# Kernel optimization log

Measured on AMD Instinct MI355X. Metric: run time of the kernel, lower is better.

The kernel has to match this reference:

```python
import jax, jax.numpy as jnp
import numpy as np

D_MODEL = 1024
NUM_HEADS = 16
BATCH = 4
SEQ = 2048


def _trunc_normal(key, shape, std):
    # truncated normal in [-3*std, 3*std], matching nn.init.trunc_normal_
    return jax.random.truncated_normal(key, -3.0, 3.0, shape, dtype=jnp.float32) * std


def setup_inputs() -> dict:
    key = jax.random.key(0)
    kx, kq, kk, kv, ko = jax.random.split(key, 5)
    std = np.sqrt(2.0 / (D_MODEL + D_MODEL)).astype(np.float32)
    x = jax.random.normal(kx, (BATCH, SEQ, D_MODEL), dtype=jnp.float32)
    # nn.Linear stores weight as [out, in]; y = x @ W.T
    W_q = _trunc_normal(kq, (D_MODEL, D_MODEL), std)
    W_k = _trunc_normal(kk, (D_MODEL, D_MODEL), std)
    W_v = _trunc_normal(kv, (D_MODEL, D_MODEL), std)
    W_o = _trunc_normal(ko, (D_MODEL, D_MODEL), std)
    return {"x": x, "W_q": W_q, "W_k": W_k, "W_v": W_v, "W_o": W_o}


def reference(x, W_q, W_k, W_v, W_o):
    b, s, d_model = x.shape
    h = NUM_HEADS
    d_k = d_model // h

    def split_heads(t):
        return t.reshape(b, s, h, d_k).transpose(0, 2, 1, 3)  # b h s d

    Q = split_heads(x @ W_q.T)
    K = split_heads(x @ W_k.T)
    V = split_heads(x @ W_v.T)

    # F.scaled_dot_product_attention with attn_mask=None -> NON-causal
    scale = 1.0 / jnp.sqrt(jnp.asarray(d_k, dtype=x.dtype))
    scores = jnp.einsum('bhqd,bhkd->bhqk', Q, K) * scale
    attn = jax.nn.softmax(scores, axis=-1)
    out = jnp.einsum('bhqk,bhkd->bhqd', attn, V)
    out = out.transpose(0, 2, 1, 3).reshape(b, s, d_model)
    return out @ W_o.T
```

## Files before the change

### kernel.cpp

```cpp
#include <hip/hip_runtime.h>
#include <hip/hip_bf16.h>
#include <stdint.h>


#define D_MODEL 1024
#define NHEAD 16
#define BATCH 4
#define SEQ 2048
#define DK 64
#define MTOT (BATCH * SEQ)

typedef __attribute__((ext_vector_type(4))) float f32x4;
typedef __attribute__((ext_vector_type(16))) float f32x16;
typedef __attribute__((ext_vector_type(8))) __bf16 bf16x8;
typedef __attribute__((ext_vector_type(8))) unsigned short ushort8;
typedef __attribute__((ext_vector_type(4))) unsigned short us4;

static __device__ __forceinline__ unsigned short f2bf(float f) {
  union { float f; unsigned int u; } v;
  v.f = f;
  unsigned int r = v.u + (0x7fffu + ((v.u >> 16) & 1u));
  return (unsigned short)(r >> 16);
}

static __device__ __forceinline__ f32x4 mfma16(bf16x8 a, bf16x8 b, f32x4 c) {
  return __builtin_amdgcn_mfma_f32_16x16x32_bf16(a, b, c, 0, 0, 0);
}
static __device__ __forceinline__ f32x16 mfma32(bf16x8 a, bf16x8 b, f32x16 c) {
  return __builtin_amdgcn_mfma_f32_32x32x16_bf16(a, b, c, 0, 0, 0);
}

static __device__ __forceinline__ unsigned int cvt_pk_bf16(float lo, float hi) {
  unsigned int r;
  asm("v_cvt_pk_bf16_f32 %0, %1, %2" : "=v"(r) : "v"(lo), "v"(hi));
  return r;
}

static __device__ __forceinline__ void gl_lds16(const void* g, void* l) {
  __builtin_amdgcn_global_load_lds((const __attribute__((address_space(1))) void*)g,
                                   (__attribute__((address_space(3))) void*)l, 16, 0, 0);
}

__global__ __launch_bounds__(256) void cvt_f32_bf16(const float* __restrict__ in,
                                                    unsigned short* __restrict__ out) {
  int i = blockIdx.x * 256 + threadIdx.x;
  f32x4 a = ((const f32x4*)in)[2 * i];
  f32x4 b = ((const f32x4*)in)[2 * i + 1];
  ushort8 r;
  r[0] = f2bf(a[0]); r[1] = f2bf(a[1]); r[2] = f2bf(a[2]); r[3] = f2bf(a[3]);
  r[4] = f2bf(b[0]); r[5] = f2bf(b[1]); r[6] = f2bf(b[2]); r[7] = f2bf(b[3]);
  ((ushort8*)out)[i] = r;
}

__global__ __launch_bounds__(256, 2) void gemm_qkv(const unsigned short* __restrict__ A,
                                                   const unsigned short* __restrict__ B3,
                                                   unsigned short* __restrict__ qh,
                                                   unsigned short* __restrict__ kh,
                                                   unsigned short* __restrict__ vtg,
                                                   float qscale) {
  __shared__ unsigned short lA[128][64];
  __shared__ unsigned short lB[128][64];
  const int t = threadIdx.x;
  const int wid = t >> 6, lane = t & 63;
  const int lr = lane & 15, lg = lane >> 4;
  const int wr = wid >> 1, wc = wid & 1;
  const int m0 = blockIdx.y * 128, n0 = blockIdx.x * 128;
  const int row8 = t >> 3, c8 = t & 7;

  f32x4 acc[4][4] = {};

  for (int kt = 0; kt < 16; ++kt) {
    const int k0 = kt * 64;
    if (kt) __syncthreads();
#pragma unroll
    for (int p = 0; p < 4; ++p) {
      gl_lds16(A  + (size_t)(m0 + p * 32 + row8) * 1024 + k0 + c8 * 8,
               &lA[0][0] + p * 2048 + t * 8);
      gl_lds16(B3 + (size_t)(n0 + p * 32 + row8) * 1024 + k0 + c8 * 8,
               &lB[0][0] + p * 2048 + t * 8);
    }
    __syncthreads();

    bf16x8 af[4][2], bfr[4][2];
#pragma unroll
    for (int rb = 0; rb < 4; ++rb)
#pragma unroll
      for (int kb = 0; kb < 2; ++kb) {
        af[rb][kb] = *(const bf16x8*)&lA[wr * 64 + rb * 16 + lr][kb * 32 + lg * 8];
        bfr[rb][kb] = *(const bf16x8*)&lB[wc * 64 + rb * 16 + lr][kb * 32 + lg * 8];
      }
    __builtin_amdgcn_s_setprio(1);
#pragma unroll
    for (int rb = 0; rb < 4; ++rb)
#pragma unroll
      for (int cb = 0; cb < 4; ++cb)
#pragma unroll
        for (int kb = 0; kb < 2; ++kb)
          acc[rb][cb] = mfma16(af[rb][kb], bfr[cb][kb], acc[rb][cb]);
    __builtin_amdgcn_s_setprio(0);
  }

  const int sel = n0 >> 10;
  const float scale = (sel == 0) ? qscale : 1.0f;
#pragma unroll
  for (int rb = 0; rb < 4; ++rb) {
    int mbase = m0 + wr * 64 + rb * 16 + lg * 4;
    int b = mbase >> 11, s0 = mbase & 2047;
#pragma unroll
    for (int cb = 0; cb < 4; ++cb) {
      int n = n0 + wc * 64 + cb * 16 + lr;
      int nl = n & 1023;
      int h = nl >> 6, d = nl & 63;
      if (sel == 2) {
        us4 v;
#pragma unroll
        for (int j = 0; j < 4; ++j) v[j] = f2bf(acc[rb][cb][j]);
        *(us4*)(vtg + ((size_t)(b * NHEAD + h) * DK + d) * SEQ + s0) = v;
      } else {
        unsigned short* out = (sel == 0) ? qh : kh;
#pragma unroll
        for (int j = 0; j < 4; ++j)
          out[((size_t)(b * NHEAD + h) * SEQ + s0 + j) * DK + d] = f2bf(acc[rb][cb][j] * scale);
      }
    }
  }
}

__global__ __launch_bounds__(256, 2) void gemm_o(const unsigned short* __restrict__ A,
                                                 const unsigned short* __restrict__ B,
                                                 float* __restrict__ out) {
  __shared__ unsigned short lA[128][64];
  __shared__ unsigned short lB[128][64];
  const int t = threadIdx.x;
  const int wid = t >> 6, lane = t & 63;
  const int lr = lane & 15, lg = lane >> 4;
  const int wr = wid >> 1, wc = wid & 1;
  const int m0 = blockIdx.y * 128, n0 = blockIdx.x * 128;
  const int row8 = t >> 3, c8 = t & 7;

  f32x4 acc[4][4] = {};

  for (int kt = 0; kt < 16; ++kt) {
    const int k0 = kt * 64;
    if (kt) __syncthreads();
#pragma unroll
    for (int p = 0; p < 4; ++p) {
      gl_lds16(A + (size_t)(m0 + p * 32 + row8) * 1024 + k0 + c8 * 8,
               &lA[0][0] + p * 2048 + t * 8);
      gl_lds16(B + (size_t)(n0 + p * 32 + row8) * 1024 + k0 + c8 * 8,
               &lB[0][0] + p * 2048 + t * 8);
    }
    __syncthreads();

    bf16x8 af[4][2], bfr[4][2];
#pragma unroll
    for (int rb = 0; rb < 4; ++rb)
#pragma unroll
      for (int kb = 0; kb < 2; ++kb) {
        af[rb][kb] = *(const bf16x8*)&lA[wr * 64 + rb * 16 + lr][kb * 32 + lg * 8];
        bfr[rb][kb] = *(const bf16x8*)&lB[wc * 64 + rb * 16 + lr][kb * 32 + lg * 8];
      }
    __builtin_amdgcn_s_setprio(1);
#pragma unroll
    for (int rb = 0; rb < 4; ++rb)
#pragma unroll
      for (int cb = 0; cb < 4; ++cb)
#pragma unroll
        for (int kb = 0; kb < 2; ++kb)
          acc[rb][cb] = mfma16(af[rb][kb], bfr[cb][kb], acc[rb][cb]);
    __builtin_amdgcn_s_setprio(0);
  }

#pragma unroll
  for (int rb = 0; rb < 4; ++rb) {
    int mbase = m0 + wr * 64 + rb * 16 + lg * 4;
#pragma unroll
    for (int cb = 0; cb < 4; ++cb) {
      int n = n0 + wc * 64 + cb * 16 + lr;
#pragma unroll
      for (int j = 0; j < 4; ++j)
        out[(size_t)(mbase + j) * 1024 + n] = acc[rb][cb][j];
    }
  }
}

__global__ __launch_bounds__(256, 2) void attn_fwd(const unsigned short* __restrict__ Qh,
                                                   const unsigned short* __restrict__ Kh,
                                                   const unsigned short* __restrict__ Vt_g,
                                                   unsigned short* __restrict__ Oout) {
  __shared__ unsigned short Kl[64 * 64];
  __shared__ unsigned short Vl[64 * 64];

  const int t = threadIdx.x;
  const int wq = t >> 6, lane = t & 63;
  const int l31 = lane & 31, hi = lane >> 5;

  const int wg = blockIdx.x;
  const int work = (wg & 7) * 64 + (wg >> 3);
  const int bh = work >> 3, qi = work & 7;
  const int q0 = qi * 256 + wq * 64;
  const size_t base = (size_t)bh * SEQ * DK;
  const int srow = t >> 3, sc = t & 7;

  bf16x8 qf0[4], qf1[4];
#pragma unroll
  for (int dt = 0; dt < 4; ++dt) {
    qf0[dt] = *(const bf16x8*)(Qh + base + (size_t)(q0 + l31) * DK + dt * 16 + hi * 8);
    qf1[dt] = *(const bf16x8*)(Qh + base + (size_t)(q0 + 32 + l31) * DK + dt * 16 + hi * 8);
  }

  f32x16 o0[2] = {}, o1[2] = {};
  float l0 = 0.f, l1 = 0.f;

  ushort8 rk0 = *(const ushort8*)(Kh + base + (size_t)srow * DK + sc * 8);
  ushort8 rk1 = *(const ushort8*)(Kh + base + (size_t)(srow + 32) * DK + sc * 8);
  ushort8 rv0 = *(const ushort8*)(Vt_g + base + (size_t)srow * SEQ + sc * 8);
  ushort8 rv1 = *(const ushort8*)(Vt_g + base + (size_t)(srow + 32) * SEQ + sc * 8);

  for (int kt = 0; kt < SEQ / 64; ++kt) {
    __syncthreads();
    {
      const int r0 = srow, r1 = srow + 32;
      *(ushort8*)((char*)Kl + ((r0 * 128 + sc * 16) ^ ((r0 & 7) << 4))) = rk0;
      *(ushort8*)((char*)Kl + ((r1 * 128 + sc * 16) ^ ((r1 & 7) << 4))) = rk1;
      *(ushort8*)((char*)Vl + ((r0 * 128 + sc * 16) ^ ((r0 & 7) << 4))) = rv0;
      *(ushort8*)((char*)Vl + ((r1 * 128 + sc * 16) ^ ((r1 & 7) << 4))) = rv1;
    }
    __syncthreads();

    if (kt < SEQ / 64 - 1) {
      const int nxt = (kt + 1) * 64;
      rk0 = *(const ushort8*)(Kh + base + (size_t)(nxt + srow) * DK + sc * 8);
      rk1 = *(const ushort8*)(Kh + base + (size_t)(nxt + srow + 32) * DK + sc * 8);
      rv0 = *(const ushort8*)(Vt_g + base + (size_t)srow * SEQ + nxt + sc * 8);
      rv1 = *(const ushort8*)(Vt_g + base + (size_t)(srow + 32) * SEQ + nxt + sc * 8);
    }

    f32x16 sS0[2] = {}, sS1[2] = {};
    __builtin_amdgcn_s_setprio(1);
#pragma unroll
    for (int kb = 0; kb < 2; ++kb) {
      const int row = kb * 32 + l31;
#pragma unroll
      for (int dt = 0; dt < 4; ++dt) {
        bf16x8 kf = *(const bf16x8*)((const char*)Kl +
                      ((row * 128 + dt * 32 + hi * 16) ^ ((row & 7) << 4)));
        sS0[kb] = mfma32(kf, qf0[dt], sS0[kb]);
        sS1[kb] = mfma32(kf, qf1[dt], sS1[kb]);
      }
    }
    __builtin_amdgcn_s_setprio(0);

    {
      float a0 = 0.f, a1 = 0.f, a2 = 0.f, a3 = 0.f;
#pragma unroll
      for (int kb = 0; kb < 2; ++kb)
#pragma unroll
        for (int r = 0; r < 16; r += 4) {
          float p0 = __builtin_amdgcn_exp2f(sS0[kb][r + 0]);
          float p1 = __builtin_amdgcn_exp2f(sS0[kb][r + 1]);
          float p2 = __builtin_amdgcn_exp2f(sS0[kb][r + 2]);
          float p3 = __builtin_amdgcn_exp2f(sS0[kb][r + 3]);
          sS0[kb][r + 0] = p0; sS0[kb][r + 1] = p1;
          sS0[kb][r + 2] = p2; sS0[kb][r + 3] = p3;
          a0 += p0; a1 += p1; a2 += p2; a3 += p3;
        }
      float ps = (a0 + a1) + (a2 + a3);
      ps += __shfl_xor(ps, 32, 64);
      l0 += ps;
    }
    {
      float a0 = 0.f, a1 = 0.f, a2 = 0.f, a3 = 0.f;
#pragma unroll
      for (int kb = 0; kb < 2; ++kb)
#pragma unroll
        for (int r = 0; r < 16; r += 4) {
          float p0 = __builtin_amdgcn_exp2f(sS1[kb][r + 0]);
          float p1 = __builtin_amdgcn_exp2f(sS1[kb][r + 1]);
          float p2 = __builtin_amdgcn_exp2f(sS1[kb][r + 2]);
          float p3 = __builtin_amdgcn_exp2f(sS1[kb][r + 3]);
          sS1[kb][r + 0] = p0; sS1[kb][r + 1] = p1;
          sS1[kb][r + 2] = p2; sS1[kb][r + 3] = p3;
          a0 += p0; a1 += p1; a2 += p2; a3 += p3;
        }
      float ps = (a0 + a1) + (a2 + a3);
      ps += __shfl_xor(ps, 32, 64);
      l1 += ps;
    }

    __builtin_amdgcn_s_setprio(1);
#pragma unroll
    for (int ks = 0; ks < 4; ++ks) {
      const int kk = ks >> 1, rb = (ks & 1) * 8;
      unsigned int a0 = cvt_pk_bf16(sS0[kk][rb + 0], sS0[kk][rb + 1]);
      unsigned int a1 = cvt_pk_bf16(sS0[kk][rb + 2], sS0[kk][rb + 3]);
      unsigned int b0 = cvt_pk_bf16(sS0[kk][rb + 4], sS0[kk][rb + 5]);
      unsigned int b1 = cvt_pk_bf16(sS0[kk][rb + 6], sS0[kk][rb + 7]);
      asm("v_permlane32_swap_b32 %0, %1" : "+v"(a0), "+v"(b0));
      asm("v_permlane32_swap_b32 %0, %1" : "+v"(a1), "+v"(b1));
      union { unsigned int u[4]; bf16x8 v; } pw0;
      pw0.u[0] = a0; pw0.u[1] = a1; pw0.u[2] = b0; pw0.u[3] = b1;

      unsigned int c0 = cvt_pk_bf16(sS1[kk][rb + 0], sS1[kk][rb + 1]);
      unsigned int c1 = cvt_pk_bf16(sS1[kk][rb + 2], sS1[kk][rb + 3]);
      unsigned int d0 = cvt_pk_bf16(sS1[kk][rb + 4], sS1[kk][rb + 5]);
      unsigned int d1 = cvt_pk_bf16(sS1[kk][rb + 6], sS1[kk][rb + 7]);
      asm("v_permlane32_swap_b32 %0, %1" : "+v"(c0), "+v"(d0));
      asm("v_permlane32_swap_b32 %0, %1" : "+v"(c1), "+v"(d1));
      union { unsigned int u[4]; bf16x8 v; } pw1;
      pw1.u[0] = c0; pw1.u[1] = c1; pw1.u[2] = d0; pw1.u[3] = d1;

#pragma unroll
      for (int dt = 0; dt < 2; ++dt) {
        const int row = dt * 32 + l31;
        bf16x8 vf = *(const bf16x8*)((const char*)Vl +
                      ((row * 128 + ks * 32 + hi * 16) ^ ((row & 7) << 4)));
        o0[dt] = mfma32(vf, pw0.v, o0[dt]);
        o1[dt] = mfma32(vf, pw1.v, o1[dt]);
      }
    }
    __builtin_amdgcn_s_setprio(0);
  }

  const int b = bh >> 4, hh = bh & 15;
  {
    const int q = q0 + l31;
    const float inv = 1.0f / l0;
    unsigned short* orow = Oout + (size_t)(b * SEQ + q) * D_MODEL + hh * 64 + hi * 4;
#pragma unroll
    for (int dt = 0; dt < 2; ++dt)
#pragma unroll
      for (int i = 0; i < 4; ++i) {
        us4 v;
#pragma unroll
        for (int j = 0; j < 4; ++j) v[j] = f2bf(o0[dt][4 * i + j] * inv);
        *(us4*)(orow + dt * 32 + 8 * i) = v;
      }
  }
  {
    const int q = q0 + 32 + l31;
    const float inv = 1.0f / l1;
    unsigned short* orow = Oout + (size_t)(b * SEQ + q) * D_MODEL + hh * 64 + hi * 4;
#pragma unroll
    for (int dt = 0; dt < 2; ++dt)
#pragma unroll
      for (int i = 0; i < 4; ++i) {
        us4 v;
#pragma unroll
        for (int j = 0; j < 4; ++j) v[j] = f2bf(o1[dt][4 * i + j] * inv);
        *(us4*)(orow + dt * 32 + 8 * i) = v;
      }
  }
}

extern "C" void kernel_launch(void* const* d_in, const int* in_sizes, int n_in,
                              void* d_out, int out_size, void* d_ws, size_t ws_size,
                              hipStream_t stream) {
  (void)in_sizes; (void)n_in; (void)out_size; (void)ws_size;
  const float* x = (const float*)d_in[0];
  const float* Wq = (const float*)d_in[1];
  const float* Wk = (const float*)d_in[2];
  const float* Wv = (const float*)d_in[3];
  const float* Wo = (const float*)d_in[4];

  char* ws = (char*)d_ws;
  unsigned short* xb   = (unsigned short*)(ws + 0);
  unsigned short* wqkv = (unsigned short*)(ws + 16777216);
  unsigned short* wob  = (unsigned short*)(ws + 23068672);
  unsigned short* qh   = (unsigned short*)(ws + 25165824);
  unsigned short* kh   = (unsigned short*)(ws + 41943040);
  unsigned short* vtg  = (unsigned short*)(ws + 58720256);
  unsigned short* at   = (unsigned short*)(ws + 75497472);

  cvt_f32_bf16<<<4096, 256, 0, stream>>>(x, xb);
  cvt_f32_bf16<<<512, 256, 0, stream>>>(Wq, wqkv);
  cvt_f32_bf16<<<512, 256, 0, stream>>>(Wk, wqkv + 1048576);
  cvt_f32_bf16<<<512, 256, 0, stream>>>(Wv, wqkv + 2097152);
  cvt_f32_bf16<<<512, 256, 0, stream>>>(Wo, wob);

  gemm_qkv<<<dim3(24, 64), 256, 0, stream>>>(xb, wqkv, qh, kh, vtg, 0.1803368801f);

  attn_fwd<<<512, 256, 0, stream>>>(qh, kh, vtg, at);

  gemm_o<<<dim3(8, 64), 256, 0, stream>>>(at, wob, (float*)d_out);
}
```

Measured before the change: 188.2 us.

## Read K/V fragments directly from global memory in attention, fuse weight conversions

Attention no longer stages K and V tiles through LDS with barriers. Each wave instead loads its MFMA fragments straight from global memory, relying on cache hits across the four waves in a block. The four weight-conversion launches become one kernel that selects its source by block index and writes into the contiguous wqkv/wob region. Both GEMMs raise their min-blocks-per-CU launch bound from 2 to 3. Dropping LDS staging removes barrier stalls, but each wave now issues redundant global loads with no software prefetch, so latency is exposed inside the inner loop.

After: 228.5 us. 1.21x slower.

```diff
diff --git a/kernel.cpp b/kernel.cpp
--- a/kernel.cpp
+++ b/kernel.cpp
@@ -52,7 +52,23 @@
   ((ushort8*)out)[i] = r;
 }
 
-__global__ __launch_bounds__(256, 2) void gemm_qkv(const unsigned short* __restrict__ A,
+__global__ __launch_bounds__(256) void cvt_w4(const float* __restrict__ wq,
+                                              const float* __restrict__ wk,
+                                              const float* __restrict__ wv,
+                                              const float* __restrict__ wo,
+                                              unsigned short* __restrict__ out) {
+  const int sel = blockIdx.x >> 9;
+  const float* in = (sel == 0) ? wq : (sel == 1) ? wk : (sel == 2) ? wv : wo;
+  int i = (blockIdx.x & 511) * 256 + threadIdx.x;
+  f32x4 a = ((const f32x4*)in)[2 * i];
+  f32x4 b = ((const f32x4*)in)[2 * i + 1];
+  ushort8 r;
+  r[0] = f2bf(a[0]); r[1] = f2bf(a[1]); r[2] = f2bf(a[2]); r[3] = f2bf(a[3]);
+  r[4] = f2bf(b[0]); r[5] = f2bf(b[1]); r[6] = f2bf(b[2]); r[7] = f2bf(b[3]);
+  ((ushort8*)(out + (size_t)sel * 1048576))[i] = r;
+}
+
+__global__ __launch_bounds__(256, 3) void gemm_qkv(const unsigned short* __restrict__ A,
                                                    const unsigned short* __restrict__ B3,
                                                    unsigned short* __restrict__ qh,
                                                    unsigned short* __restrict__ kh,
@@ -126,7 +142,7 @@
   }
 }
 
-__global__ __launch_bounds__(256, 2) void gemm_o(const unsigned short* __restrict__ A,
+__global__ __launch_bounds__(256, 3) void gemm_o(const unsigned short* __restrict__ A,
                                                  const unsigned short* __restrict__ B,
                                                  float* __restrict__ out) {
   __shared__ unsigned short lA[128][64];
@@ -188,9 +204,6 @@
                                                    const unsigned short* __restrict__ Kh,
                                                    const unsigned short* __restrict__ Vt_g,
                                                    unsigned short* __restrict__ Oout) {
-  __shared__ unsigned short Kl[64 * 64];
-  __shared__ unsigned short Vl[64 * 64];
-
   const int t = threadIdx.x;
   const int wq = t >> 6, lane = t & 63;
   const int l31 = lane & 31, hi = lane >> 5;
@@ -200,7 +213,6 @@
   const int bh = work >> 3, qi = work & 7;
   const int q0 = qi * 256 + wq * 64;
   const size_t base = (size_t)bh * SEQ * DK;
-  const int srow = t >> 3, sc = t & 7;
 
   bf16x8 qf0[4], qf1[4];
 #pragma unroll
@@ -212,39 +224,20 @@
   f32x16 o0[2] = {}, o1[2] = {};
   float l0 = 0.f, l1 = 0.f;
 
-  ushort8 rk0 = *(const ushort8*)(Kh + base + (size_t)srow * DK + sc * 8);
-  ushort8 rk1 = *(const ushort8*)(Kh + base + (size_t)(srow + 32) * DK + sc * 8);
-  ushort8 rv0 = *(const ushort8*)(Vt_g + base + (size_t)srow * SEQ + sc * 8);
-  ushort8 rv1 = *(const ushort8*)(Vt_g + base + (size_t)(srow + 32) * SEQ + sc * 8);
+  const unsigned short* Kb = Kh + base;
+  const unsigned short* Vb = Vt_g + base;
 
   for (int kt = 0; kt < SEQ / 64; ++kt) {
-    __syncthreads();
-    {
-      const int r0 = srow, r1 = srow + 32;
-      *(ushort8*)((char*)Kl + ((r0 * 128 + sc * 16) ^ ((r0 & 7) << 4))) = rk0;
-      *(ushort8*)((char*)Kl + ((r1 * 128 + sc * 16) ^ ((r1 & 7) << 4))) = rk1;
-      *(ushort8*)((char*)Vl + ((r0 * 128 + sc * 16) ^ ((r0 & 7) << 4))) = rv0;
-      *(ushort8*)((char*)Vl + ((r1 * 128 + sc * 16) ^ ((r1 & 7) << 4))) = rv1;
-    }
-    __syncthreads();
-
-    if (kt < SEQ / 64 - 1) {
-      const int nxt = (kt + 1) * 64;
-      rk0 = *(const ushort8*)(Kh + base + (size_t)(nxt + srow) * DK + sc * 8);
-      rk1 = *(const ushort8*)(Kh + base + (size_t)(nxt + srow + 32) * DK + sc * 8);
-      rv0 = *(const ushort8*)(Vt_g + base + (size_t)srow * SEQ + nxt + sc * 8);
-      rv1 = *(const ushort8*)(Vt_g + base + (size_t)(srow + 32) * SEQ + nxt + sc * 8);
-    }
+    const int s0 = kt * 64;
 
     f32x16 sS0[2] = {}, sS1[2] = {};
     __builtin_amdgcn_s_setprio(1);
 #pragma unroll
     for (int kb = 0; kb < 2; ++kb) {
-      const int row = kb * 32 + l31;
+      const int krow = s0 + kb * 32 + l31;
 #pragma unroll
       for (int dt = 0; dt < 4; ++dt) {
-        bf16x8 kf = *(const bf16x8*)((const char*)Kl +
-                      ((row * 128 + dt * 32 + hi * 16) ^ ((row & 7) << 4)));
+        bf16x8 kf = *(const bf16x8*)(Kb + (size_t)krow * DK + dt * 16 + hi * 8);
         sS0[kb] = mfma32(kf, qf0[dt], sS0[kb]);
         sS1[kb] = mfma32(kf, qf1[dt], sS1[kb]);
       }
@@ -312,9 +305,8 @@
 
 #pragma unroll
       for (int dt = 0; dt < 2; ++dt) {
-        const int row = dt * 32 + l31;
-        bf16x8 vf = *(const bf16x8*)((const char*)Vl +
-                      ((row * 128 + ks * 32 + hi * 16) ^ ((row & 7) << 4)));
+        const int d = dt * 32 + l31;
+        bf16x8 vf = *(const bf16x8*)(Vb + (size_t)d * SEQ + s0 + ks * 16 + hi * 8);
         o0[dt] = mfma32(vf, pw0.v, o0[dt]);
         o1[dt] = mfma32(vf, pw1.v, o1[dt]);
       }
@@ -373,10 +365,7 @@
   unsigned short* at   = (unsigned short*)(ws + 75497472);
 
   cvt_f32_bf16<<<4096, 256, 0, stream>>>(x, xb);
-  cvt_f32_bf16<<<512, 256, 0, stream>>>(Wq, wqkv);
-  cvt_f32_bf16<<<512, 256, 0, stream>>>(Wk, wqkv + 1048576);
-  cvt_f32_bf16<<<512, 256, 0, stream>>>(Wv, wqkv + 2097152);
-  cvt_f32_bf16<<<512, 256, 0, stream>>>(Wo, wob);
+  cvt_w4<<<2048, 256, 0, stream>>>(Wq, Wk, Wv, Wo, wqkv);
 
   gemm_qkv<<<dim3(24, 64), 256, 0, stream>>>(xb, wqkv, qh, kh, vtg, 0.1803368801f);
 
```
